# Kernel tuning notes

Measured on AMD Instinct MI355X. Metric: run time of the kernel, lower is better.

## Reference

```python
import jax, jax.numpy as jnp
import numpy as np

N = 100000
IN_DIM = 128
OUT_DIM = 128
E = 3200000


def setup_inputs() -> dict:
    key = jax.random.key(0)
    k1, k2, k3, k4, k5 = jax.random.split(key, 5)
    x = jax.random.normal(k1, (N, IN_DIM), dtype=jnp.float32)
    src = jax.random.randint(k2, (E,), 0, N)
    dst = jax.random.randint(k3, (E,), 0, N)
    edge_index = jnp.stack([src, dst], axis=0)  # (2, E) int
    # Linear(2*in_dim, out_dim): torch stores weight as (out, in)
    bound = 1.0 / np.sqrt(2 * IN_DIM)
    W = jax.random.uniform(k4, (OUT_DIM, 2 * IN_DIM), minval=-bound, maxval=bound, dtype=jnp.float32)
    b = jax.random.uniform(k5, (OUT_DIM,), minval=-bound, maxval=bound, dtype=jnp.float32)
    return {"x": x, "edge_index": edge_index, "W": W, "b": b}


def reference(x, edge_index, W, b):
    # x: (N, d), edge_index: (2, E)
    n = x.shape[0]
    src, dst = edge_index[0], edge_index[1]
    # scatter-add of source features into target buckets (mean aggregation)
    agg = jax.ops.segment_sum(x[src], dst, num_segments=n)          # (N, d)
    count = jax.ops.segment_sum(jnp.ones((src.shape[0],), x.dtype), dst, num_segments=n)
    count = jnp.maximum(count, 1.0)[:, None]                         # (N, 1)
    neigh_mean = agg / count
    combined = jnp.concatenate([x, neigh_mean], axis=1)              # (N, 2d)
    return combined @ W.T + b
```

## Files before the change

### kernel.cpp

```cpp
#include <hip/hip_runtime.h>

typedef unsigned int u32;
typedef unsigned short u16;
typedef __bf16 bf16x8 __attribute__((ext_vector_type(8)));
typedef float f32x4 __attribute__((ext_vector_type(4)));
typedef float f32x2 __attribute__((ext_vector_type(2)));

__device__ __forceinline__ u16 f2bf(float f) {
  u32 u = __builtin_bit_cast(u32, f);
  u32 r = (u + 0x7fffu + ((u >> 16) & 1u)) >> 16;
  return (u16)r;
}

__global__ __launch_bounds__(256) void pre_k(const float* __restrict__ x, u16* __restrict__ xbf,
                                             u32* __restrict__ xq,
                                             const float* __restrict__ W, u16* __restrict__ wbf,
                                             u32* __restrict__ bktTotal, int N, int nbkt,
                                             int nbx, int nbz) {
  int b = blockIdx.x, tid = threadIdx.x;
  if (b < nbx) {
    int i = b * 256 + tid;
    if (i < N * 32) {
      const float4 v = *(const float4*)(x + (size_t)i * 4);
      ushort4 o = { f2bf(v.x), f2bf(v.y), f2bf(v.z), f2bf(v.w) };
      *(ushort4*)(xbf + (size_t)i * 4) = o;
      u32 p = 0;
      p = __builtin_amdgcn_cvt_pk_fp8_f32(v.x, v.y, p, false);
      p = __builtin_amdgcn_cvt_pk_fp8_f32(v.z, v.w, p, true);
      xq[i] = p;
    }
  } else if (b < nbx + nbz) {
    int i = (b - nbx) * 256 + tid;
    if (i < nbkt) bktTotal[i] = 0u;
  } else {
    int i = (b - nbx - nbz) * 256 + tid;
    if (i < 8192) {
      const float4 v = *(const float4*)(W + (size_t)i * 4);
      ushort4 o = { f2bf(v.x), f2bf(v.y), f2bf(v.z), f2bf(v.w) };
      *(ushort4*)(wbf + (size_t)i * 4) = o;
    }
  }
}

__global__ __launch_bounds__(256) void hist_k(const int* __restrict__ dst, int E,
                                              u32* __restrict__ bktTotal, int nbkt) {
  __shared__ u32 h[512];
  for (int t = threadIdx.x; t < 512; t += 256) h[t] = 0u;
  __syncthreads();
  int base = blockIdx.x * 8192;
  for (int it = 0; it < 32; it++) {
    int i = base + it * 256 + threadIdx.x;
    if (i < E) atomicAdd(&h[(u32)dst[i] >> 8], 1u);
  }
  __syncthreads();
  for (int t = threadIdx.x; t < nbkt; t += 256) {
    u32 c = h[t];
    if (c) atomicAdd(&bktTotal[t], c);
  }
}

__global__ __launch_bounds__(512) void bscan_k(const u32* __restrict__ bktTotal, int nbkt,
                                               int E, int N, u32* __restrict__ start,
                                               u32* __restrict__ cursor, u32* __restrict__ offsets) {
  __shared__ u32 s[512];
  int t = threadIdx.x;
  u32 v = (t < nbkt) ? bktTotal[t] : 0u;
  s[t] = v;
  __syncthreads();
  for (int off = 1; off < 512; off <<= 1) {
    u32 x = (t >= off) ? s[t - off] : 0u;
    __syncthreads();
    s[t] += x;
    __syncthreads();
  }
  u32 excl = s[t] - v;
  if (t < nbkt) { start[t] = excl; cursor[t] = excl; }
  if (t == nbkt - 1) start[nbkt] = excl + v;
  if (t == 0) offsets[N] = (u32)E;
}

__global__ __launch_bounds__(256) void part_k(const int* __restrict__ src, const int* __restrict__ dst,
                                              int E, u32* __restrict__ cursor,
                                              u32* __restrict__ packed, int nbkt) {
  __shared__ u32 h[512];
  for (int t = threadIdx.x; t < 512; t += 256) h[t] = 0u;
  __syncthreads();
  int base = blockIdx.x * 8192;
  for (int it = 0; it < 32; it++) {
    int i = base + it * 256 + threadIdx.x;
    if (i < E) atomicAdd(&h[(u32)dst[i] >> 8], 1u);
  }
  __syncthreads();
  for (int t = threadIdx.x; t < nbkt; t += 256) {
    u32 c = h[t];
    h[t] = c ? atomicAdd(&cursor[t], c) : 0u;
  }
  __syncthreads();
  for (int it = 0; it < 32; it++) {
    int i = base + it * 256 + threadIdx.x;
    if (i < E) {
      u32 d = (u32)dst[i];
      u32 pos = atomicAdd(&h[d >> 8], 1u);
      packed[pos] = (u32)src[i] | ((d & 255u) << 24);
    }
  }
}

__global__ __launch_bounds__(256) void bucket_k(const u32* __restrict__ packed,
                                                const u32* __restrict__ start, int N,
                                                u32* __restrict__ offsets, int* __restrict__ ssrc) {
  __shared__ u32 cnt[256];
  __shared__ u32 scn[256];
  __shared__ u32 cur[256];
  int b = blockIdx.x, t = threadIdx.x;
  u32 lo = start[b], hi = start[b + 1];
  cnt[t] = 0u;
  __syncthreads();
  for (u32 j = lo + t; j < hi; j += 256) atomicAdd(&cnt[packed[j] >> 24], 1u);
  __syncthreads();
  u32 v = cnt[t];
  scn[t] = v;
  __syncthreads();
  for (int off = 1; off < 256; off <<= 1) {
    u32 x = (t >= off) ? scn[t - off] : 0u;
    __syncthreads();
    scn[t] += x;
    __syncthreads();
  }
  u32 base = lo + scn[t] - v;
  int node = b * 256 + t;
  if (node < N) offsets[node] = base;
  cur[t] = base;
  __syncthreads();
  for (u32 j = lo + t; j < hi; j += 256) {
    u32 w = packed[j];
    u32 pos = atomicAdd(&cur[w >> 24], 1u);
    ssrc[pos] = (int)(w & 0xFFFFFFu);
  }
}

#define DEC8(vv) { f32x2 p;                                             \
    p = __builtin_amdgcn_cvt_pk_f32_fp8((vv).x, false); a0 += p.x; a1 += p.y; \
    p = __builtin_amdgcn_cvt_pk_f32_fp8((vv).x, true);  a2 += p.x; a3 += p.y; \
    p = __builtin_amdgcn_cvt_pk_f32_fp8((vv).y, false); a4 += p.x; a5 += p.y; \
    p = __builtin_amdgcn_cvt_pk_f32_fp8((vv).y, true);  a6 += p.x; a7 += p.y; }

__global__ __launch_bounds__(256) void fuse_k(const int* __restrict__ ssrc,
                                              const u32* __restrict__ offsets,
                                              const u32* __restrict__ xq,
                                              const u16* __restrict__ xbf,
                                              const u16* __restrict__ wbf,
                                              const float* __restrict__ bias,
                                              float* __restrict__ out, int N) {
  __shared__ u16 mlds[64][136];
  int wv = threadIdx.x >> 6, lane = threadIdx.x & 63;
  int sub = lane >> 4, cl = lane & 15;
  int wbase = blockIdx.x * 64 + wv * 16;

  for (int r = 0; r < 4; r++) {
    int ln = r * 4 + sub;
    int node = wbase + ln;
    float a0=0.f,a1=0.f,a2=0.f,a3=0.f,a4=0.f,a5=0.f,a6=0.f,a7=0.f;
    u32 deg = 0;
    if (node < N) {
      u32 s0 = offsets[node], s1 = offsets[node + 1];
      deg = s1 - s0;
      u32 j = s0;
      for (; j + 3 < s1; j += 4) {
        int e0 = ssrc[j], e1 = ssrc[j + 1], e2 = ssrc[j + 2], e3 = ssrc[j + 3];
        uint2 v0 = *(const uint2*)(xq + ((size_t)e0 << 5) + (cl << 1));
        uint2 v1 = *(const uint2*)(xq + ((size_t)e1 << 5) + (cl << 1));
        uint2 v2 = *(const uint2*)(xq + ((size_t)e2 << 5) + (cl << 1));
        uint2 v3 = *(const uint2*)(xq + ((size_t)e3 << 5) + (cl << 1));
        DEC8(v0) DEC8(v1) DEC8(v2) DEC8(v3)
      }
      for (; j < s1; j++) {
        int e = ssrc[j];
        uint2 v = *(const uint2*)(xq + ((size_t)e << 5) + (cl << 1));
        DEC8(v)
      }
    }
    float inv = 1.0f / (float)(deg ? deg : 1u);
    uint4 o;
    o.x = (u32)f2bf(a0 * inv) | ((u32)f2bf(a1 * inv) << 16);
    o.y = (u32)f2bf(a2 * inv) | ((u32)f2bf(a3 * inv) << 16);
    o.z = (u32)f2bf(a4 * inv) | ((u32)f2bf(a5 * inv) << 16);
    o.w = (u32)f2bf(a6 * inv) | ((u32)f2bf(a7 * inv) << 16);
    *(uint4*)&mlds[wv * 16 + ln][cl * 8] = o;
  }
  __syncthreads();

  int la = cl, lb = sub;
  bf16x8 a[8];
  const u16* ab = xbf + ((size_t)(wbase + la) << 7) + lb * 8;
#pragma unroll
  for (int kb = 0; kb < 4; kb++) a[kb] = *(const bf16x8*)(ab + kb * 32);
#pragma unroll
  for (int kb = 0; kb < 4; kb++) a[4 + kb] = *(const bf16x8*)(&mlds[wv * 16 + la][kb * 32 + lb * 8]);

#pragma unroll
  for (int ct = 0; ct < 8; ct++) {
    f32x4 acc = { 0.f, 0.f, 0.f, 0.f };
    const u16* bbase = wbf + ((size_t)(ct * 16 + la) << 8) + lb * 8;
#pragma unroll
    for (int kb = 0; kb < 8; kb++) {
      bf16x8 b = *(const bf16x8*)(bbase + kb * 32);
      acc = __builtin_amdgcn_mfma_f32_16x16x32_bf16(a[kb], b, acc, 0, 0, 0);
    }
    float bc = bias[ct * 16 + la];
#pragma unroll
    for (int j = 0; j < 4; j++) {
      int r = wbase + lb * 4 + j;
      if (r < N) out[((size_t)r << 7) + ct * 16 + la] = acc[j] + bc;
    }
  }
}

extern "C" void kernel_launch(void* const* d_in, const int* in_sizes, int n_in,
                              void* d_out, int out_size, void* d_ws, size_t ws_size,
                              hipStream_t stream) {
  const float* x    = (const float*)d_in[0];
  const int*   ei   = (const int*)d_in[1];
  const float* W    = (const float*)d_in[2];
  const float* bias = (const float*)d_in[3];
  const int N = in_sizes[0] / 128;
  const int E = in_sizes[1] / 2;
  const int nbkt = (N + 255) >> 8;
  const int* src = ei;
  const int* dst = ei + E;
  float* out = (float*)d_out;

  u32* packed   = (u32*)d_out;
  u32* bktTotal = packed + E;
  u32* start    = bktTotal + nbkt;
  u32* cursor   = start + nbkt + 1;

  char* ws = (char*)d_ws;
  u32* offsets = (u32*)ws;
  size_t off = ((size_t)(N + 1) * 4 + 255) & ~(size_t)255;
  int* ssrc = (int*)(ws + off);
  off += (size_t)E * 4;
  off = (off + 255) & ~(size_t)255;
  u16* xbf = (u16*)(ws + off);
  off += (size_t)N * 128 * 2;
  off = (off + 255) & ~(size_t)255;
  u32* xq = (u32*)(ws + off);
  off += (size_t)N * 128;
  off = (off + 255) & ~(size_t)255;
  u16* wbf = (u16*)(ws + off);

  const int nbx = (N * 32 + 255) / 256;
  const int nbz = (nbkt + 255) / 256;
  const int nba = (E + 8191) / 8192;
  pre_k<<<nbx + nbz + 32, 256, 0, stream>>>(x, xbf, xq, W, wbf, bktTotal, N, nbkt, nbx, nbz);
  hist_k<<<nba, 256, 0, stream>>>(dst, E, bktTotal, nbkt);
  bscan_k<<<1, 512, 0, stream>>>(bktTotal, nbkt, E, N, start, cursor, offsets);
  part_k<<<nba, 256, 0, stream>>>(src, dst, E, cursor, packed, nbkt);
  bucket_k<<<nbkt, 256, 0, stream>>>(packed, start, N, offsets, ssrc);
  fuse_k<<<(N + 63) / 64, 256, 0, stream>>>(ssrc, offsets, xq, xbf, wbf, bias, out, N);
}
```

Baseline: 211.9 us.

## Sort nodes by degree within groups to balance gather work across wavefronts

Measured after the change: 210.0 us. About the same (-0.9%).

```diff
diff --git a/kernel.cpp b/kernel.cpp
--- a/kernel.cpp
+++ b/kernel.cpp
@@ -2,6 +2,7 @@
 
 typedef unsigned int u32;
 typedef unsigned short u16;
+typedef unsigned char u8;
 typedef __bf16 bf16x8 __attribute__((ext_vector_type(8)));
 typedef float f32x4 __attribute__((ext_vector_type(4)));
 typedef float f32x2 __attribute__((ext_vector_type(2)));
@@ -108,7 +109,8 @@
 
 __global__ __launch_bounds__(256) void bucket_k(const u32* __restrict__ packed,
                                                 const u32* __restrict__ start, int N,
-                                                u32* __restrict__ offsets, int* __restrict__ ssrc) {
+                                                u32* __restrict__ offsets, int* __restrict__ ssrc,
+                                                u8* __restrict__ nodeperm) {
   __shared__ u32 cnt[256];
   __shared__ u32 scn[256];
   __shared__ u32 cur[256];
@@ -137,13 +139,25 @@
     u32 pos = atomicAdd(&cur[w >> 24], 1u);
     ssrc[pos] = (int)(w & 0xFFFFFFu);
   }
-}
-
-#define DEC8(vv) { f32x2 p;                                             \
-    p = __builtin_amdgcn_cvt_pk_f32_fp8((vv).x, false); a0 += p.x; a1 += p.y; \
-    p = __builtin_amdgcn_cvt_pk_f32_fp8((vv).x, true);  a2 += p.x; a3 += p.y; \
-    p = __builtin_amdgcn_cvt_pk_f32_fp8((vv).y, false); a4 += p.x; a5 += p.y; \
-    p = __builtin_amdgcn_cvt_pk_f32_fp8((vv).y, true);  a6 += p.x; a7 += p.y; }
+  {
+    int g = t >> 6, l = t & 63;
+    u32 mykey = cnt[t] * 256u + (u32)l;
+    const u32* cg = &cnt[g * 64];
+    u32 rank = 0;
+#pragma unroll 8
+    for (int l2 = 0; l2 < 64; l2++) {
+      u32 k2 = cg[l2] * 256u + (u32)l2;
+      rank += (k2 < mykey) ? 1u : 0u;
+    }
+    nodeperm[(size_t)b * 256 + g * 64 + rank] = (u8)l;
+  }
+}
+
+#define DECV(vv, A0, A1, A2, A3) { f32x2 p;                              \
+    p = __builtin_amdgcn_cvt_pk_f32_fp8((vv).x, false); A0 += p;         \
+    p = __builtin_amdgcn_cvt_pk_f32_fp8((vv).x, true);  A1 += p;         \
+    p = __builtin_amdgcn_cvt_pk_f32_fp8((vv).y, false); A2 += p;         \
+    p = __builtin_amdgcn_cvt_pk_f32_fp8((vv).y, true);  A3 += p; }
 
 __global__ __launch_bounds__(256) void fuse_k(const int* __restrict__ ssrc,
                                               const u32* __restrict__ offsets,
@@ -151,46 +165,68 @@
                                               const u16* __restrict__ xbf,
                                               const u16* __restrict__ wbf,
                                               const float* __restrict__ bias,
+                                              const u8* __restrict__ nodeperm,
                                               float* __restrict__ out, int N) {
   __shared__ u16 mlds[64][136];
   int wv = threadIdx.x >> 6, lane = threadIdx.x & 63;
   int sub = lane >> 4, cl = lane & 15;
-  int wbase = blockIdx.x * 64 + wv * 16;
+  int nbase = blockIdx.x * 64;
+
+  int pidx[4];
+#pragma unroll
+  for (int r = 0; r < 4; r++)
+    pidx[r] = nodeperm[(size_t)nbase + r * 16 + wv * 4 + sub];
 
   for (int r = 0; r < 4; r++) {
-    int ln = r * 4 + sub;
-    int node = wbase + ln;
-    float a0=0.f,a1=0.f,a2=0.f,a3=0.f,a4=0.f,a5=0.f,a6=0.f,a7=0.f;
+    int ln = pidx[r];
+    int node = nbase + ln;
+    f32x2 A0{0.f,0.f}, A1{0.f,0.f}, A2{0.f,0.f}, A3{0.f,0.f};
     u32 deg = 0;
     if (node < N) {
       u32 s0 = offsets[node], s1 = offsets[node + 1];
       deg = s1 - s0;
       u32 j = s0;
-      for (; j + 3 < s1; j += 4) {
-        int e0 = ssrc[j], e1 = ssrc[j + 1], e2 = ssrc[j + 2], e3 = ssrc[j + 3];
-        uint2 v0 = *(const uint2*)(xq + ((size_t)e0 << 5) + (cl << 1));
-        uint2 v1 = *(const uint2*)(xq + ((size_t)e1 << 5) + (cl << 1));
-        uint2 v2 = *(const uint2*)(xq + ((size_t)e2 << 5) + (cl << 1));
-        uint2 v3 = *(const uint2*)(xq + ((size_t)e3 << 5) + (cl << 1));
-        DEC8(v0) DEC8(v1) DEC8(v2) DEC8(v3)
+      u32 nq = deg >> 2;
+      if (nq) {
+        uint4 iA = *(const uint4*)(ssrc + j);
+        for (u32 q = 1; q < nq; q++) {
+          uint4 iN = *(const uint4*)(ssrc + j + 4);
+          uint2 v0 = *(const uint2*)(xq + ((size_t)iA.x << 5) + (cl << 1));
+          uint2 v1 = *(const uint2*)(xq + ((size_t)iA.y << 5) + (cl << 1));
+          uint2 v2 = *(const uint2*)(xq + ((size_t)iA.z << 5) + (cl << 1));
+          uint2 v3 = *(const uint2*)(xq + ((size_t)iA.w << 5) + (cl << 1));
+          DECV(v0, A0, A1, A2, A3) DECV(v1, A0, A1, A2, A3)
+          DECV(v2, A0, A1, A2, A3) DECV(v3, A0, A1, A2, A3)
+          iA = iN; j += 4;
+        }
+        {
+          uint2 v0 = *(const uint2*)(xq + ((size_t)iA.x << 5) + (cl << 1));
+          uint2 v1 = *(const uint2*)(xq + ((size_t)iA.y << 5) + (cl << 1));
+          uint2 v2 = *(const uint2*)(xq + ((size_t)iA.z << 5) + (cl << 1));
+          uint2 v3 = *(const uint2*)(xq + ((size_t)iA.w << 5) + (cl << 1));
+          DECV(v0, A0, A1, A2, A3) DECV(v1, A0, A1, A2, A3)
+          DECV(v2, A0, A1, A2, A3) DECV(v3, A0, A1, A2, A3)
+          j += 4;
+        }
       }
       for (; j < s1; j++) {
         int e = ssrc[j];
         uint2 v = *(const uint2*)(xq + ((size_t)e << 5) + (cl << 1));
-        DEC8(v)
+        DECV(v, A0, A1, A2, A3)
       }
     }
     float inv = 1.0f / (float)(deg ? deg : 1u);
     uint4 o;
-    o.x = (u32)f2bf(a0 * inv) | ((u32)f2bf(a1 * inv) << 16);
-    o.y = (u32)f2bf(a2 * inv) | ((u32)f2bf(a3 * inv) << 16);
-    o.z = (u32)f2bf(a4 * inv) | ((u32)f2bf(a5 * inv) << 16);
-    o.w = (u32)f2bf(a6 * inv) | ((u32)f2bf(a7 * inv) << 16);
-    *(uint4*)&mlds[wv * 16 + ln][cl * 8] = o;
+    o.x = (u32)f2bf(A0.x * inv) | ((u32)f2bf(A0.y * inv) << 16);
+    o.y = (u32)f2bf(A1.x * inv) | ((u32)f2bf(A1.y * inv) << 16);
+    o.z = (u32)f2bf(A2.x * inv) | ((u32)f2bf(A2.y * inv) << 16);
+    o.w = (u32)f2bf(A3.x * inv) | ((u32)f2bf(A3.y * inv) << 16);
+    *(uint4*)&mlds[ln][cl * 8] = o;
   }
   __syncthreads();
 
   int la = cl, lb = sub;
+  int wbase = nbase + wv * 16;
   bf16x8 a[8];
   const u16* ab = xbf + ((size_t)(wbase + la) << 7) + lb * 8;
 #pragma unroll
@@ -248,6 +284,9 @@
   off += (size_t)N * 128;
   off = (off + 255) & ~(size_t)255;
   u16* wbf = (u16*)(ws + off);
+  off += (size_t)128 * 256 * 2;
+  off = (off + 255) & ~(size_t)255;
+  u8* nodeperm = (u8*)(ws + off);
 
   const int nbx = (N * 32 + 255) / 256;
   const int nbz = (nbkt + 255) / 256;
@@ -256,6 +295,6 @@
   hist_k<<<nba, 256, 0, stream>>>(dst, E, bktTotal, nbkt);
   bscan_k<<<1, 512, 0, stream>>>(bktTotal, nbkt, E, N, start, cursor, offsets);
   part_k<<<nba, 256, 0, stream>>>(src, dst, E, cursor, packed, nbkt);
-  bucket_k<<<nbkt, 256, 0, stream>>>(packed, start, N, offsets, ssrc);
-  fuse_k<<<(N + 63) / 64, 256, 0, stream>>>(ssrc, offsets, xq, xbf, wbf, bias, out, N);
-}
+  bucket_k<<<nbkt, 256, 0, stream>>>(packed, start, N, offsets, ssrc, nodeperm);
+  fuse_k<<<(N + 63) / 64, 256, 0, stream>>>(ssrc, offsets, xq, xbf, wbf, bias, nodeperm, out, N);
+}
```
